# Kernel tuning notes

Measured on AMD Instinct MI355X. Metric: run time of the kernel, lower is better.

Reference implementation:

```python
import jax, jax.numpy as jnp
import numpy as np

N = 100000      # nodes
E = 1600000     # directed edges (before self loops)
F_IN = 3        # node_feature_dim
H = 32          # hidden_dim
BN_EPS = 1e-5


def _linear_params(k, fan_in, fan_out):
    lim = 1.0 / np.sqrt(fan_in)
    kw, kb = jax.random.split(k)
    W = jax.random.uniform(kw, (fan_in, fan_out), jnp.float32, -lim, lim)
    b = jax.random.uniform(kb, (fan_out,), jnp.float32, -lim, lim)
    return W, b


def setup_inputs() -> dict:
    key = jax.random.key(0)
    ks = jax.random.split(key, 12)
    x = jax.random.normal(ks[0], (N, F_IN), jnp.float32)
    edge_index = jax.random.randint(ks[1], (2, E), 0, N, dtype=jnp.int64)
    node_type = jax.random.randint(ks[2], (N,), 0, 3, dtype=jnp.int64)
    W1, b1 = _linear_params(ks[3], F_IN, H)
    W2, b2 = _linear_params(ks[4], H, H)
    W3, b3 = _linear_params(ks[5], H, H)
    g1 = jnp.ones((H,), jnp.float32); be1 = jnp.zeros((H,), jnp.float32)
    g2 = jnp.ones((H,), jnp.float32); be2 = jnp.zeros((H,), jnp.float32)
    Wc1, bc1 = _linear_params(ks[6], H, H // 2)
    Wc2, bc2 = _linear_params(ks[7], H // 2, 1)
    Wd1, bd1 = _linear_params(ks[8], H, H // 2)
    Wd2, bd2 = _linear_params(ks[9], H // 2, 1)
    return dict(x=x, edge_index=edge_index, node_type=node_type,
                W1=W1, b1=b1, W2=W2, b2=b2, W3=W3, b3=b3,
                g1=g1, be1=be1, g2=g2, be2=be2,
                Wc1=Wc1, bc1=bc1, Wc2=Wc2, bc2=bc2,
                Wd1=Wd1, bd1=bd1, Wd2=Wd2, bd2=bd2)


def reference(x, edge_index, node_type, W1, b1, W2, b2, W3, b3,
              g1, be1, g2, be2, Wc1, bc1, Wc2, bc2, Wd1, bd1, Wd2, bd2):
    n = x.shape[0]
    # GCNConv (PyG default): add self loops, symmetric deg^-1/2 normalization
    loop = jnp.arange(n, dtype=edge_index.dtype)
    src = jnp.concatenate([edge_index[0], loop])  # [E+N]
    dst = jnp.concatenate([edge_index[1], loop])
    deg = jax.ops.segment_sum(jnp.ones_like(dst, dtype=x.dtype), dst, num_segments=n)
    dinv = jnp.where(deg > 0, jax.lax.rsqrt(jnp.maximum(deg, 1.0)), 0.0)
    norm = dinv[src] * dinv[dst]  # [E+N]

    def conv(h, W, b):
        msg = (h @ W)[src] * norm[:, None]                  # gather + scale
        return jax.ops.segment_sum(msg, dst, num_segments=n) + b  # scatter-add

    def bn(h, g, be):  # BatchNorm1d with batch statistics (training math)
        mu = h.mean(axis=0)
        var = ((h - mu) ** 2).mean(axis=0)
        return (h - mu) * jax.lax.rsqrt(var + BN_EPS) * g + be

    h = bn(jax.nn.relu(conv(x, W1, b1)), g1, be1)   # dropout = identity (eval)
    h = bn(jax.nn.relu(conv(h, W2, b2)), g2, be2)
    h = jax.nn.relu(conv(h, W3, b3))

    cand_mask = node_type == 0
    cand_emb = h[cand_mask]                                 # [C, H]
    cand_scores = (jax.nn.relu(cand_emb @ Wc1 + bc1) @ Wc2 + bc2)[:, 0]

    w = jax.nn.softmax(h.sum(axis=1))[:, None]              # [N,1] importance
    g_emb = (h * w).sum(axis=0, keepdims=True)              # [1, H]
    dn = (jax.nn.relu(g_emb @ Wd1 + bd1) @ Wd2 + bd2).reshape(())

    logits = jnp.concatenate([cand_scores, dn[None]], axis=0)
    cand_idx = jnp.nonzero(cand_mask)[0]
    return logits, cand_idx
```

## Files before the change

kernel.cpp:

```cpp
#include <hip/hip_runtime.h>
#include <hip/hip_bf16.h>

typedef unsigned int uint;
typedef unsigned short ushort;

#define NB_MAX 256
#define NPB_MAX 2048

static __device__ __forceinline__ ushort f2b(float f) {
    uint u = __float_as_uint(f);
    uint r = (u + 0x7FFFu + ((u >> 16) & 1u)) >> 16;
    return (ushort)r;
}
static __device__ __forceinline__ float b2f_u(ushort h) { return __uint_as_float(((uint)h) << 16); }

static __device__ __forceinline__ void unpack8(uint4 v, float* o) {
    o[0] = b2f_u(v.x & 0xFFFF); o[1] = b2f_u(v.x >> 16);
    o[2] = b2f_u(v.y & 0xFFFF); o[3] = b2f_u(v.y >> 16);
    o[4] = b2f_u(v.z & 0xFFFF); o[5] = b2f_u(v.z >> 16);
    o[6] = b2f_u(v.w & 0xFFFF); o[7] = b2f_u(v.w >> 16);
}

static __device__ __forceinline__ unsigned wave_incl_scan(unsigned v) {
    int lane = threadIdx.x & 63;
    #pragma unroll
    for (int d = 1; d < 64; d <<= 1) {
        unsigned t = (unsigned)__shfl_up((int)v, d, 64);
        if (lane >= d) v += t;
    }
    return v;
}

static __device__ void block_excl_scan(const uint* in, uint* out, int n, uint* wscr) {
    int tid = threadIdx.x;
    int lane = tid & 63, wid = tid >> 6;
    int base = tid * 8;
    uint v[8], pre[8], s = 0;
    #pragma unroll
    for (int k = 0; k < 8; k++) v[k] = (base + k < n) ? in[base + k] : 0u;
    #pragma unroll
    for (int k = 0; k < 8; k++) { pre[k] = s; s += v[k]; }
    uint is = wave_incl_scan(s);
    __syncthreads();
    if (lane == 63) wscr[wid] = is;
    __syncthreads();
    uint woff = 0;
    for (int wI = 0; wI < wid; wI++) woff += wscr[wI];
    uint excl = is - s + woff;
    #pragma unroll
    for (int k = 0; k < 8; k++) if (base + k < n) out[base + k] = excl + pre[k];
    __syncthreads();
}

__global__ __launch_bounds__(256) void bucket_hist_kernel(const int* src, const int* dst,
                                                          const int* nt, uint* bcnt, uint* bcand,
                                                          int E, int N, int NB, int shift) {
    __shared__ uint bh[NB_MAX], ch[NB_MAX];
    int tid = threadIdx.x;
    bh[tid] = 0; ch[tid] = 0;
    __syncthreads();
    int gs = gridDim.x * 256;
    for (int i = blockIdx.x * 256 + tid; i < E; i += gs) {
        int d = dst[i], s = src[i];
        if ((uint)d < (uint)N && (uint)s < (uint)N) atomicAdd(&bh[d >> shift], 1u);
    }
    for (int i = blockIdx.x * 256 + tid; i < N; i += gs) {
        if (nt[i] == 0) atomicAdd(&ch[i >> shift], 1u);
    }
    __syncthreads();
    if (bh[tid]) atomicAdd(&bcnt[tid], bh[tid]);
    if (ch[tid]) atomicAdd(&bcand[tid], ch[tid]);
}

__global__ __launch_bounds__(256) void partition_kernel(const int* src, const int* dst,
                                                        const uint* bcnt, uint* alloc0,
                                                        uint* staging, int E, int N, int shift) {
    __shared__ uint bbase_s[NB_MAX];
    __shared__ uint lh[NB_MAX], gb[NB_MAX];
    __shared__ uint ws4[4];
    int tid = threadIdx.x;
    int lane = tid & 63, wid = tid >> 6;
    uint a = bcnt[tid];
    uint ia = wave_incl_scan(a);
    if (lane == 63) ws4[wid] = ia;
    __syncthreads();
    uint off = 0;
    for (int wI = 0; wI < wid; wI++) off += ws4[wI];
    bbase_s[tid] = ia - a + off;
    lh[tid] = 0;
    __syncthreads();
    int base = blockIdx.x * 2048;
    uint mask = (1u << shift) - 1u;
    int sreg[8], breg[8];
    uint rreg[8], dlreg[8];
    #pragma unroll
    for (int k = 0; k < 8; k++) {
        int e = base + k * 256 + tid;
        breg[k] = -1;
        if (e < E) {
            int s = src[e], d = dst[e];
            if ((uint)d < (uint)N && (uint)s < (uint)N) {
                int b = d >> shift;
                sreg[k] = s; dlreg[k] = (uint)d & mask; breg[k] = b;
                rreg[k] = atomicAdd(&lh[b], 1u);
            }
        }
    }
    __syncthreads();
    gb[tid] = lh[tid] ? (bbase_s[tid] + atomicAdd(&alloc0[tid], lh[tid])) : 0u;
    __syncthreads();
    #pragma unroll
    for (int k = 0; k < 8; k++) {
        if (breg[k] >= 0)
            staging[gb[breg[k]] + rreg[k]] = (dlreg[k] << 17) | (uint)sreg[k];
    }
}

__global__ __launch_bounds__(256) void local_csr_kernel(const uint* staging, const uint* bcnt,
                                                        const uint* bcand, const int* nt,
                                                        const float* x, const float* W1,
                                                        int* csr_src, uint* csr_off, uint* cand_pos,
                                                        float* dinv, ushort* zb,
                                                        int N, int shift, int NB) {
    __shared__ uint deg[NPB_MAX];
    __shared__ uint ofs[NPB_MAX];
    __shared__ uint ws4[4];
    __shared__ uint sb[4];
    __shared__ float Ws[96];
    int b = blockIdx.x, tid = threadIdx.x;
    int lane = tid & 63, wid = tid >> 6;
    if (tid < 96) Ws[tid] = W1[tid];
    uint a = bcnt[tid];
    uint ia = wave_incl_scan(a);
    if (lane == 63) ws4[wid] = ia;
    __syncthreads();
    uint off = 0;
    for (int wI = 0; wI < wid; wI++) off += ws4[wI];
    if (tid == b) { sb[0] = ia - a + off; sb[1] = ia + off; }
    __syncthreads();
    uint c = bcand[tid];
    uint ic = wave_incl_scan(c);
    if (lane == 63) ws4[wid] = ic;
    __syncthreads();
    uint offc = 0;
    for (int wI = 0; wI < wid; wI++) offc += ws4[wI];
    if (tid == b) sb[2] = ic - c + offc;
    __syncthreads();
    uint ebase = sb[0], eend = sb[1], cb = sb[2];
    int nbase = b << shift;
    int ncount = min(1 << shift, N - nbase);
    for (int i = tid; i < ncount; i += 256) deg[i] = 0;
    __syncthreads();
    for (uint p = ebase + tid; p < eend; p += 256)
        atomicAdd(&deg[staging[p] >> 17], 1u);
    __syncthreads();
    block_excl_scan(deg, ofs, ncount, ws4);
    for (int i = tid; i < ncount; i += 256)
        csr_off[nbase + i] = ebase + ofs[i];
    if (b == NB - 1 && tid == 0) csr_off[N] = eend;
    for (int i = tid; i < ncount; i += 256) {
        int g = nbase + i;
        float di = rsqrtf((float)(deg[i] + 1u));
        dinv[g] = di;
        float x0 = x[3 * g], x1 = x[3 * g + 1], x2 = x[3 * g + 2];
        uint pk[16];
        #pragma unroll
        for (int q = 0; q < 16; q++) {
            int j0 = 2 * q, j1 = 2 * q + 1;
            float o0 = (x0 * Ws[j0] + x1 * Ws[32 + j0] + x2 * Ws[64 + j0]) * di;
            float o1 = (x0 * Ws[j1] + x1 * Ws[32 + j1] + x2 * Ws[64 + j1]) * di;
            pk[q] = (uint)f2b(o0) | ((uint)f2b(o1) << 16);
        }
        uint4* zp = (uint4*)(zb + (size_t)g * 32);
        #pragma unroll
        for (int r = 0; r < 4; r++) zp[r] = make_uint4(pk[4*r], pk[4*r+1], pk[4*r+2], pk[4*r+3]);
    }
    __syncthreads();
    for (int i = tid; i < ncount; i += 256) deg[i] = 0;
    __syncthreads();
    for (uint p = ebase + tid; p < eend; p += 256) {
        uint pkv = staging[p];
        uint dl = pkv >> 17;
        uint pos = ebase + ofs[dl] + atomicAdd(&deg[dl], 1u);
        csr_src[pos] = (int)(pkv & 0x1FFFFu);
    }
    __syncthreads();
    for (int i = tid; i < ncount; i += 256) deg[i] = (nt[nbase + i] == 0) ? 1u : 0u;
    __syncthreads();
    block_excl_scan(deg, ofs, ncount, ws4);
    for (int i = tid; i < ncount; i += 256) cand_pos[nbase + i] = cb + ofs[i];
}

__global__ __launch_bounds__(256) void gemmf_kernel(const ushort* hb, const float* stats_sum,
                                                    const float* stats_sq, const float* g,
                                                    const float* be, const float* W,
                                                    const float* dinv, ushort* zb, int n,
                                                    float inv_n) {
    __shared__ float Ws[1024];
    __shared__ float cs[32];
    __shared__ float a_s[32], d_s[32];
    int tid = threadIdx.x;
    if (tid < 32) {
        float mu = stats_sum[tid] * inv_n;
        float var = fmaxf(stats_sq[tid] * inv_n - mu * mu, 0.f);
        float a = g[tid] * rsqrtf(var + 1e-5f);
        a_s[tid] = a;
        d_s[tid] = be[tid] - mu * a;
    }
    __syncthreads();
    #pragma unroll
    for (int t = tid; t < 1024; t += 256) Ws[t] = a_s[t >> 5] * W[t];
    if (tid < 32) {
        float c = 0.f;
        for (int k = 0; k < 32; k++) c += d_s[k] * W[k * 32 + tid];
        cs[tid] = c;
    }
    __syncthreads();
    int i = blockIdx.x * 256 + tid;
    if (i >= n) return;
    const uint4* hp = (const uint4*)(hb + (size_t)i * 32);
    float hk[32];
    #pragma unroll
    for (int r = 0; r < 4; r++) unpack8(hp[r], hk + r * 8);
    float acc[32];
    #pragma unroll
    for (int j = 0; j < 32; j++) acc[j] = cs[j];
    #pragma unroll
    for (int k = 0; k < 32; k++) {
        float h0 = hk[k];
        #pragma unroll
        for (int j = 0; j < 32; j++) acc[j] += h0 * Ws[k * 32 + j];
    }
    float di = dinv[i];
    uint pk[16];
    #pragma unroll
    for (int q = 0; q < 16; q++)
        pk[q] = (uint)f2b(acc[2*q] * di) | ((uint)f2b(acc[2*q+1] * di) << 16);
    uint4* zp = (uint4*)(zb + (size_t)i * 32);
    #pragma unroll
    for (int r = 0; r < 4; r++) zp[r] = make_uint4(pk[4*r], pk[4*r+1], pk[4*r+2], pk[4*r+3]);
}

__global__ __launch_bounds__(256) void agg_kernel(const ushort* zb, const int* csr_src,
                                                  const uint* csr_off, const float* dinv,
                                                  const float* bias, ushort* hb, int n,
                                                  int mode, float* stats_sum, float* stats_sq,
                                                  float* rowsum, uint* maxkey) {
    const int tid = threadIdx.x;
    const int wave = tid >> 6;
    const int lane = tid & 63;
    const int c4 = lane & 3;
    const int slot = lane >> 2;
    float bs[8], bq[8];
    #pragma unroll
    for (int j = 0; j < 8; j++) { bs[j] = 0.f; bq[j] = 0.f; }
    float lmax = -3.0e38f;
    int node = (blockIdx.x * 4 + wave) * 16 + slot;
    if (node < n) {
        uint s = csr_off[node], e = csr_off[node + 1];
        float acc[8];
        unpack8(*(const uint4*)(zb + (size_t)node * 32 + c4 * 8), acc);
        for (uint p = s; p < e; p += 8) {
            uint idx[8];
            float wg[8];
            #pragma unroll
            for (int j = 0; j < 8; j++) {
                uint q = p + (uint)j;
                uint qc = min(q, e - 1u);
                idx[j] = (uint)csr_src[qc];
                wg[j] = (q < e) ? 1.f : 0.f;
            }
            #pragma unroll
            for (int j = 0; j < 8; j++) {
                float t[8];
                unpack8(*(const uint4*)(zb + (size_t)idx[j] * 32 + c4 * 8), t);
                #pragma unroll
                for (int cI = 0; cI < 8; cI++) acc[cI] = fmaf(wg[j], t[cI], acc[cI]);
            }
        }
        float di = dinv[node];
        float hv[8];
        #pragma unroll
        for (int j = 0; j < 8; j++) hv[j] = fmaxf(di * acc[j] + bias[c4 * 8 + j], 0.f);
        uint4 o;
        o.x = (uint)f2b(hv[0]) | ((uint)f2b(hv[1]) << 16);
        o.y = (uint)f2b(hv[2]) | ((uint)f2b(hv[3]) << 16);
        o.z = (uint)f2b(hv[4]) | ((uint)f2b(hv[5]) << 16);
        o.w = (uint)f2b(hv[6]) | ((uint)f2b(hv[7]) << 16);
        *(uint4*)(hb + (size_t)node * 32 + c4 * 8) = o;
        if (mode == 0) {
            #pragma unroll
            for (int j = 0; j < 8; j++) { bs[j] = hv[j]; bq[j] = hv[j] * hv[j]; }
        } else {
            float rs = ((hv[0] + hv[1]) + (hv[2] + hv[3])) + ((hv[4] + hv[5]) + (hv[6] + hv[7]));
            rs += __shfl_xor(rs, 1, 64);
            rs += __shfl_xor(rs, 2, 64);
            if (c4 == 0) { rowsum[node] = rs; lmax = rs; }
        }
    }
    if (mode == 0) {
        #pragma unroll
        for (int m = 4; m < 64; m <<= 1) {
            #pragma unroll
            for (int j = 0; j < 8; j++) {
                bs[j] += __shfl_xor(bs[j], m, 64);
                bq[j] += __shfl_xor(bq[j], m, 64);
            }
        }
        __shared__ float ssum[4][32], ssq[4][32];
        if (slot == 0) {
            #pragma unroll
            for (int j = 0; j < 8; j++) { ssum[wave][c4 * 8 + j] = bs[j]; ssq[wave][c4 * 8 + j] = bq[j]; }
        }
        __syncthreads();
        if (tid < 32) {
            atomicAdd(&stats_sum[tid], ssum[0][tid] + ssum[1][tid] + ssum[2][tid] + ssum[3][tid]);
            atomicAdd(&stats_sq[tid],  ssq[0][tid] + ssq[1][tid] + ssq[2][tid] + ssq[3][tid]);
        }
    } else {
        #pragma unroll
        for (int m = 1; m < 64; m <<= 1) lmax = fmaxf(lmax, __shfl_xor(lmax, m, 64));
        __shared__ float lm[4];
        if (lane == 0) lm[wave] = lmax;
        __syncthreads();
        if (tid == 0) {
            float m = fmaxf(fmaxf(lm[0], lm[1]), fmaxf(lm[2], lm[3]));
            uint u = __float_as_uint(m);
            uint key = (u & 0x80000000u) ? ~u : (u | 0x80000000u);
            atomicMax(maxkey, key);
        }
    }
}

__global__ __launch_bounds__(256) void head_kernel(const ushort* hb, const int* nt,
                                                   const uint* pos, const float* Wc1,
                                                   const float* bc1, const float* Wc2,
                                                   const float* bc2, const float* rowsum,
                                                   const uint* maxkey, float* gvec, float* Zp,
                                                   uint* ticket, const float* Wd1,
                                                   const float* bd1, const float* Wd2,
                                                   const float* bd2, float* out, int n, int C) {
    __shared__ float W1s[512], b1s[16], W2s[16];
    __shared__ float ls[256];
    __shared__ float ge[32], tt[16];
    __shared__ int lastflag;
    int tid = threadIdx.x;
    for (int t = tid; t < 512; t += 256) W1s[t] = Wc1[t];
    if (tid < 16) { b1s[tid] = bc1[tid]; W2s[tid] = Wc2[tid]; }
    __syncthreads();
    int i = blockIdx.x * 256 + tid;
    if (i < n && nt[i] == 0) {
        const uint4* hp = (const uint4*)(hb + (size_t)i * 32);
        float hv[32];
        #pragma unroll
        for (int r = 0; r < 4; r++) unpack8(hp[r], hv + r * 8);
        float s = bc2[0];
        #pragma unroll
        for (int j = 0; j < 16; j++) {
            float u = b1s[j];
            #pragma unroll
            for (int k = 0; k < 32; k++) u += hv[k] * W1s[k * 16 + j];
            s += fmaxf(u, 0.f) * W2s[j];
        }
        s = fminf(fmaxf(s, -1000.f), 1000.f);
        uint p = pos[i];
        if (p < (uint)C) {
            out[p] = s;
            out[C + 1 + p] = (float)i;
        }
    }
    uint key = *maxkey;
    float M = 0.f;
    if (key != 0u) M = (key & 0x80000000u) ? __uint_as_float(key ^ 0x80000000u) : __uint_as_float(~key);
    int lane = tid & 31, grp = tid >> 5;
    int stride = gridDim.x * 8;
    float accZ = 0.f, accg = 0.f;
    for (int node = blockIdx.x * 8 + grp; node < n; node += stride) {
        float ew = __expf(rowsum[node] - M);
        accg += b2f_u(hb[(size_t)node * 32 + lane]) * ew;
        if (lane == 0) accZ += ew;
    }
    ls[tid] = accg;
    __syncthreads();
    if (tid < 32) {
        float a = 0.f;
        #pragma unroll
        for (int g = 0; g < 8; g++) a += ls[tid + 32 * g];
        atomicAdd(&gvec[tid], a);
    }
    __syncthreads();
    ls[tid] = (lane == 0) ? accZ : 0.f;
    __syncthreads();
    if (tid == 0) {
        float a = 0.f;
        for (int t = 0; t < 256; t += 32) a += ls[t];
        atomicAdd(Zp, a);
        __threadfence();
        uint old = atomicAdd(ticket, 1u);
        lastflag = (old == gridDim.x - 1) ? 1 : 0;
    }
    __syncthreads();
    if (lastflag) {
        __threadfence();
        if (tid < 32) ge[tid] = atomicAdd(&gvec[tid], 0.f);
        if (tid == 0) ls[0] = atomicAdd(Zp, 0.f);
        __syncthreads();
        float Zv = fmaxf(ls[0], 1e-30f);
        if (tid < 32) ge[tid] /= Zv;
        __syncthreads();
        if (tid < 16) {
            float s = bd1[tid];
            for (int k = 0; k < 32; k++) s += ge[k] * Wd1[k * 16 + tid];
            tt[tid] = fmaxf(s, 0.f);
        }
        __syncthreads();
        if (tid == 0) {
            float s = bd2[0];
            for (int j = 0; j < 16; j++) s += tt[j] * Wd2[j];
            out[C] = fminf(fmaxf(s, -1000.f), 1000.f);
        }
    }
}

extern "C" void kernel_launch(void* const* d_in, const int* in_sizes, int n_in,
                              void* d_out, int out_size, void* d_ws, size_t ws_size,
                              hipStream_t stream) {
    const float* x   = (const float*)d_in[0];
    const int*   ei  = (const int*)d_in[1];
    const int*   nt  = (const int*)d_in[2];
    const float* W1  = (const float*)d_in[3];  const float* b1  = (const float*)d_in[4];
    const float* W2  = (const float*)d_in[5];  const float* b2  = (const float*)d_in[6];
    const float* W3  = (const float*)d_in[7];  const float* b3  = (const float*)d_in[8];
    const float* g1  = (const float*)d_in[9];  const float* be1 = (const float*)d_in[10];
    const float* g2  = (const float*)d_in[11]; const float* be2 = (const float*)d_in[12];
    const float* Wc1 = (const float*)d_in[13]; const float* bc1 = (const float*)d_in[14];
    const float* Wc2 = (const float*)d_in[15]; const float* bc2 = (const float*)d_in[16];
    const float* Wd1 = (const float*)d_in[17]; const float* bd1 = (const float*)d_in[18];
    const float* Wd2 = (const float*)d_in[19]; const float* bd2 = (const float*)d_in[20];

    const int N = in_sizes[0] / 3;
    const int E = in_sizes[1] / 2;
    const int C = (out_size - 1) / 2;
    const int* e_src = ei;
    const int* e_dst = ei + E;
    float* out = (float*)d_out;

    int shift = 9;
    while (((N + (1 << shift) - 1) >> shift) > NB_MAX) shift++;
    const int NB = (N + (1 << shift) - 1) >> shift;

    char* w = (char*)d_ws;
    auto alloc = [&](size_t bytes) { void* p = (void*)w; w += (bytes + 255) & ~(size_t)255; return p; };
    float*    stats  = (float*)alloc(256 * 4);
    uint*     bcnt   = (uint*)alloc(NB_MAX * 4);
    uint*     bcand  = (uint*)alloc(NB_MAX * 4);
    uint*     alloc0 = (uint*)alloc(NB_MAX * 4);
    size_t zero_bytes = (size_t)((char*)w - (char*)stats);
    float*    dinv   = (float*)alloc((size_t)N * 4);
    uint*     csr_off= (uint*)alloc((size_t)(N + 1) * 4);
    uint*     cand_pos=(uint*)alloc((size_t)N * 4);
    float*    rowsum = (float*)alloc((size_t)N * 4);
    int*      csr_src= (int*)alloc((size_t)E * 4);
    ushort*   zb     = (ushort*)alloc((size_t)N * 32 * 2);
    ushort*   hb     = (ushort*)alloc((size_t)N * 32 * 2);
    uint*     staging = (uint*)hb;

    float* sum1 = stats;       float* sq1 = stats + 32;
    float* sum2 = stats + 64;  float* sq2 = stats + 96;
    float* gvec = stats + 128; float* Zp  = stats + 160;
    uint* maxkey = (uint*)(stats + 161);
    uint* ticket = (uint*)(stats + 162);

    hipMemsetAsync(stats, 0, zero_bytes, stream);

    const int gN   = (N + 255) / 256;
    const int gPar = (E + 2047) / 2048;
    const int gAgg = (N + 63) / 64;
    const float inv_n = 1.0f / (float)N;

    hipLaunchKernelGGL(bucket_hist_kernel, dim3(784), dim3(256), 0, stream, e_src, e_dst, nt, bcnt, bcand, E, N, NB, shift);
    hipLaunchKernelGGL(partition_kernel, dim3(gPar), dim3(256), 0, stream, e_src, e_dst, bcnt, alloc0, staging, E, N, shift);
    hipLaunchKernelGGL(local_csr_kernel, dim3(NB), dim3(256), 0, stream, staging, bcnt, bcand, nt,
                       x, W1, csr_src, csr_off, cand_pos, dinv, zb, N, shift, NB);

    hipLaunchKernelGGL(agg_kernel, dim3(gAgg), dim3(256), 0, stream, zb, csr_src, csr_off,
                       dinv, b1, hb, N, 0, sum1, sq1, rowsum, maxkey);

    hipLaunchKernelGGL(gemmf_kernel, dim3(gN), dim3(256), 0, stream, hb, sum1, sq1, g1, be1, W2, dinv, zb, N, inv_n);
    hipLaunchKernelGGL(agg_kernel, dim3(gAgg), dim3(256), 0, stream, zb, csr_src, csr_off,
                       dinv, b2, hb, N, 0, sum2, sq2, rowsum, maxkey);

    hipLaunchKernelGGL(gemmf_kernel, dim3(gN), dim3(256), 0, stream, hb, sum2, sq2, g2, be2, W3, dinv, zb, N, inv_n);
    hipLaunchKernelGGL(agg_kernel, dim3(gAgg), dim3(256), 0, stream, zb, csr_src, csr_off,
                       dinv, b3, hb, N, 1, sum1, sq1, rowsum, maxkey);

    hipLaunchKernelGGL(head_kernel, dim3(gN), dim3(256), 0, stream, hb, nt, cand_pos,
                       Wc1, bc1, Wc2, bc2, rowsum, maxkey, gvec, Zp, ticket,
                       Wd1, bd1, Wd2, bd2, out, N, C);
}
```

Measured before the change: 369.0 us.

## Fuse pipeline into cooperative persistent megakernel and store features as fp8

Replaces the sequence of separate kernels with a single cooperative-launched persistent kernel that runs every phase, separated by grid-wide syncs, with a multi-kernel fallback. Node feature buffers change from bf16 to a software-encoded e4m3-style fp8 format, halving gather traffic during aggregation. Staging gets its own buffer instead of aliasing hb, and the bucket scan is done once instead of per block. This removes launch gaps and memory traffic, but fp8 adds precision loss and grid syncs may leave cores idle between phases.

```diff
diff --git a/kernel.cpp b/kernel.cpp
--- a/kernel.cpp
+++ b/kernel.cpp
@@ -1,36 +1,80 @@
 #include <hip/hip_runtime.h>
-#include <hip/hip_bf16.h>
+#include <hip/hip_cooperative_groups.h>
 
 typedef unsigned int uint;
-typedef unsigned short ushort;
-
-#define NB_MAX 256
-#define NPB_MAX 2048
-
-static __device__ __forceinline__ ushort f2b(float f) {
-    uint u = __float_as_uint(f);
-    uint r = (u + 0x7FFFu + ((u >> 16) & 1u)) >> 16;
-    return (ushort)r;
-}
-static __device__ __forceinline__ float b2f_u(ushort h) { return __uint_as_float(((uint)h) << 16); }
-
-static __device__ __forceinline__ void unpack8(uint4 v, float* o) {
-    o[0] = b2f_u(v.x & 0xFFFF); o[1] = b2f_u(v.x >> 16);
-    o[2] = b2f_u(v.y & 0xFFFF); o[3] = b2f_u(v.y >> 16);
-    o[4] = b2f_u(v.z & 0xFFFF); o[5] = b2f_u(v.z >> 16);
-    o[6] = b2f_u(v.w & 0xFFFF); o[7] = b2f_u(v.w >> 16);
-}
-
-static __device__ __forceinline__ unsigned wave_incl_scan(unsigned v) {
+typedef unsigned char uchar;
+
+namespace cg = cooperative_groups;
+
+#define SMW 4300
+
+static __device__ __forceinline__ uint f2fp8(float v) {
+    v = fminf(fmaxf(v, -448.f), 448.f);
+    uint u = __float_as_uint(v);
+    uint s = (u >> 24) & 0x80u;
+    uint mag = u & 0x7FFFFFFFu;
+    uint r = mag + 0x7FFFFu + ((mag >> 20) & 1u);
+    if (r < 0x3C800000u) return s;
+    uint e8 = (r - 0x3C000000u) >> 20;
+    return s | min(e8, 0x7Eu);
+}
+static __device__ __forceinline__ float fp82f(uint b) {
+    uint mag = b & 0x7Fu;
+    uint bits = ((b & 0x80u) << 24) | ((mag << 20) + 0x3C000000u);
+    return mag ? __uint_as_float(bits) : 0.f;
+}
+static __device__ __forceinline__ void dec8(uint2 v, float* o) {
+    o[0]=fp82f(v.x&0xFF); o[1]=fp82f((v.x>>8)&0xFF); o[2]=fp82f((v.x>>16)&0xFF); o[3]=fp82f(v.x>>24);
+    o[4]=fp82f(v.y&0xFF); o[5]=fp82f((v.y>>8)&0xFF); o[6]=fp82f((v.y>>16)&0xFF); o[7]=fp82f(v.y>>24);
+}
+static __device__ __forceinline__ uint2 enc8(const float* o) {
+    uint2 r;
+    r.x = f2fp8(o[0]) | (f2fp8(o[1])<<8) | (f2fp8(o[2])<<16) | (f2fp8(o[3])<<24);
+    r.y = f2fp8(o[4]) | (f2fp8(o[5])<<8) | (f2fp8(o[6])<<16) | (f2fp8(o[7])<<24);
+    return r;
+}
+static __device__ __forceinline__ void dec32(const uchar* row, float* o) {
+    const uint4* r4 = (const uint4*)row;
+    uint4 A = r4[0], B = r4[1];
+    dec8(make_uint2(A.x,A.y), o); dec8(make_uint2(A.z,A.w), o+8);
+    dec8(make_uint2(B.x,B.y), o+16); dec8(make_uint2(B.z,B.w), o+24);
+}
+static __device__ __forceinline__ void enc32(const float* o, uchar* row) {
+    uint2 a = enc8(o), b = enc8(o+8), c = enc8(o+16), d = enc8(o+24);
+    uint4* r4 = (uint4*)row;
+    r4[0] = make_uint4(a.x,a.y,b.x,b.y);
+    r4[1] = make_uint4(c.x,c.y,d.x,d.y);
+}
+
+struct GP {
+    const float* x; const int* esrc; const int* edst; const int* nt;
+    const float* W1; const float* b1; const float* W2; const float* b2;
+    const float* W3; const float* b3; const float* g1; const float* be1;
+    const float* g2; const float* be2;
+    const float* Wc1; const float* bc1; const float* Wc2; const float* bc2;
+    const float* Wd1; const float* bd1; const float* Wd2; const float* bd2;
+    float* stats;
+    uint* bcnt; uint* bcand; uint* alloc0;
+    uint* bbase; uint* cbase;
+    float* dinv; uint* csr_off; uint* cand_pos; float* rowsum;
+    int* csr_src; uint* staging;
+    uchar* zb; uchar* hb;
+    float* sum1; float* sq1; float* sum2; float* sq2;
+    float* gvec; float* Zp; uint* maxkey;
+    float* out;
+    int N, E, C, NB, shift, nCh;
+    float inv_n;
+};
+
+static __device__ __forceinline__ uint wave_incl_scan(uint v) {
     int lane = threadIdx.x & 63;
     #pragma unroll
     for (int d = 1; d < 64; d <<= 1) {
-        unsigned t = (unsigned)__shfl_up((int)v, d, 64);
+        uint t = (uint)__shfl_up((int)v, d, 64);
         if (lane >= d) v += t;
     }
     return v;
 }
-
 static __device__ void block_excl_scan(const uint* in, uint* out, int n, uint* wscr) {
     int tid = threadIdx.x;
     int lane = tid & 63, wid = tid >> 6;
@@ -52,252 +96,231 @@
     __syncthreads();
 }
 
-__global__ __launch_bounds__(256) void bucket_hist_kernel(const int* src, const int* dst,
-                                                          const int* nt, uint* bcnt, uint* bcand,
-                                                          int E, int N, int NB, int shift) {
-    __shared__ uint bh[NB_MAX], ch[NB_MAX];
+static __device__ void ph_zero(const GP& p) {
+    if (blockIdx.x != 0) return;
+    uint* z = (uint*)p.stats;
+    for (int i = threadIdx.x; i < 1024; i += 256) z[i] = 0u;
+}
+
+static __device__ void ph_hist(const GP& p, uint* sm) {
+    uint* bh = sm; uint* ch = sm + 256;
     int tid = threadIdx.x;
     bh[tid] = 0; ch[tid] = 0;
     __syncthreads();
     int gs = gridDim.x * 256;
-    for (int i = blockIdx.x * 256 + tid; i < E; i += gs) {
-        int d = dst[i], s = src[i];
-        if ((uint)d < (uint)N && (uint)s < (uint)N) atomicAdd(&bh[d >> shift], 1u);
-    }
-    for (int i = blockIdx.x * 256 + tid; i < N; i += gs) {
-        if (nt[i] == 0) atomicAdd(&ch[i >> shift], 1u);
-    }
-    __syncthreads();
-    if (bh[tid]) atomicAdd(&bcnt[tid], bh[tid]);
-    if (ch[tid]) atomicAdd(&bcand[tid], ch[tid]);
-}
-
-__global__ __launch_bounds__(256) void partition_kernel(const int* src, const int* dst,
-                                                        const uint* bcnt, uint* alloc0,
-                                                        uint* staging, int E, int N, int shift) {
-    __shared__ uint bbase_s[NB_MAX];
-    __shared__ uint lh[NB_MAX], gb[NB_MAX];
-    __shared__ uint ws4[4];
-    int tid = threadIdx.x;
-    int lane = tid & 63, wid = tid >> 6;
-    uint a = bcnt[tid];
-    uint ia = wave_incl_scan(a);
-    if (lane == 63) ws4[wid] = ia;
-    __syncthreads();
-    uint off = 0;
-    for (int wI = 0; wI < wid; wI++) off += ws4[wI];
-    bbase_s[tid] = ia - a + off;
-    lh[tid] = 0;
-    __syncthreads();
-    int base = blockIdx.x * 2048;
-    uint mask = (1u << shift) - 1u;
-    int sreg[8], breg[8];
-    uint rreg[8], dlreg[8];
-    #pragma unroll
-    for (int k = 0; k < 8; k++) {
-        int e = base + k * 256 + tid;
-        breg[k] = -1;
-        if (e < E) {
-            int s = src[e], d = dst[e];
-            if ((uint)d < (uint)N && (uint)s < (uint)N) {
-                int b = d >> shift;
-                sreg[k] = s; dlreg[k] = (uint)d & mask; breg[k] = b;
-                rreg[k] = atomicAdd(&lh[b], 1u);
+    for (int i = blockIdx.x * 256 + tid; i < p.E; i += gs) {
+        int d = p.edst[i], s = p.esrc[i];
+        if ((uint)d < (uint)p.N && (uint)s < (uint)p.N) atomicAdd(&bh[d >> p.shift], 1u);
+    }
+    for (int i = blockIdx.x * 256 + tid; i < p.N; i += gs)
+        if (p.nt[i] == 0) atomicAdd(&ch[i >> p.shift], 1u);
+    __syncthreads();
+    if (bh[tid]) atomicAdd(&p.bcnt[tid], bh[tid]);
+    if (ch[tid]) atomicAdd(&p.bcand[tid], ch[tid]);
+}
+
+static __device__ void ph_bscan(const GP& p, uint* sm) {
+    if (blockIdx.x != 0) return;
+    int tid = threadIdx.x, lane = tid & 63, wid = tid >> 6;
+    uint* ws4 = sm;
+    {
+        uint a = p.bcnt[tid];
+        uint ia = wave_incl_scan(a);
+        if (lane == 63) ws4[wid] = ia;
+        __syncthreads();
+        uint off = 0;
+        for (int wI = 0; wI < wid; wI++) off += ws4[wI];
+        p.bbase[tid] = ia - a + off;
+        if (tid == 255) p.bbase[256] = ia + off;
+        __syncthreads();
+    }
+    {
+        uint a = p.bcand[tid];
+        uint ia = wave_incl_scan(a);
+        if (lane == 63) ws4[wid] = ia;
+        __syncthreads();
+        uint off = 0;
+        for (int wI = 0; wI < wid; wI++) off += ws4[wI];
+        p.cbase[tid] = ia - a + off;
+        if (tid == 255) p.cbase[256] = ia + off;
+        __syncthreads();
+    }
+}
+
+static __device__ void ph_part(const GP& p, uint* sm) {
+    uint* lh = sm; uint* gb = sm + 256;
+    int tid = threadIdx.x;
+    uint mask = (1u << p.shift) - 1u;
+    for (int chunk = blockIdx.x; chunk < p.nCh; chunk += gridDim.x) {
+        lh[tid] = 0;
+        __syncthreads();
+        int base = chunk << 11;
+        int breg[8]; uint rreg[8], pk8[8];
+        #pragma unroll
+        for (int k = 0; k < 8; k++) {
+            int e = base + k * 256 + tid;
+            breg[k] = -1;
+            if (e < p.E) {
+                int s = p.esrc[e], d = p.edst[e];
+                if ((uint)d < (uint)p.N && (uint)s < (uint)p.N) {
+                    int b = d >> p.shift;
+                    pk8[k] = (((uint)d & mask) << 17) | (uint)s;
+                    breg[k] = b;
+                    rreg[k] = atomicAdd(&lh[b], 1u);
+                }
             }
         }
-    }
-    __syncthreads();
-    gb[tid] = lh[tid] ? (bbase_s[tid] + atomicAdd(&alloc0[tid], lh[tid])) : 0u;
-    __syncthreads();
-    #pragma unroll
-    for (int k = 0; k < 8; k++) {
-        if (breg[k] >= 0)
-            staging[gb[breg[k]] + rreg[k]] = (dlreg[k] << 17) | (uint)sreg[k];
-    }
-}
-
-__global__ __launch_bounds__(256) void local_csr_kernel(const uint* staging, const uint* bcnt,
-                                                        const uint* bcand, const int* nt,
-                                                        const float* x, const float* W1,
-                                                        int* csr_src, uint* csr_off, uint* cand_pos,
-                                                        float* dinv, ushort* zb,
-                                                        int N, int shift, int NB) {
-    __shared__ uint deg[NPB_MAX];
-    __shared__ uint ofs[NPB_MAX];
-    __shared__ uint ws4[4];
-    __shared__ uint sb[4];
-    __shared__ float Ws[96];
-    int b = blockIdx.x, tid = threadIdx.x;
-    int lane = tid & 63, wid = tid >> 6;
-    if (tid < 96) Ws[tid] = W1[tid];
-    uint a = bcnt[tid];
-    uint ia = wave_incl_scan(a);
-    if (lane == 63) ws4[wid] = ia;
-    __syncthreads();
-    uint off = 0;
-    for (int wI = 0; wI < wid; wI++) off += ws4[wI];
-    if (tid == b) { sb[0] = ia - a + off; sb[1] = ia + off; }
-    __syncthreads();
-    uint c = bcand[tid];
-    uint ic = wave_incl_scan(c);
-    if (lane == 63) ws4[wid] = ic;
-    __syncthreads();
-    uint offc = 0;
-    for (int wI = 0; wI < wid; wI++) offc += ws4[wI];
-    if (tid == b) sb[2] = ic - c + offc;
-    __syncthreads();
-    uint ebase = sb[0], eend = sb[1], cb = sb[2];
-    int nbase = b << shift;
-    int ncount = min(1 << shift, N - nbase);
-    for (int i = tid; i < ncount; i += 256) deg[i] = 0;
-    __syncthreads();
-    for (uint p = ebase + tid; p < eend; p += 256)
-        atomicAdd(&deg[staging[p] >> 17], 1u);
-    __syncthreads();
-    block_excl_scan(deg, ofs, ncount, ws4);
-    for (int i = tid; i < ncount; i += 256)
-        csr_off[nbase + i] = ebase + ofs[i];
-    if (b == NB - 1 && tid == 0) csr_off[N] = eend;
-    for (int i = tid; i < ncount; i += 256) {
-        int g = nbase + i;
-        float di = rsqrtf((float)(deg[i] + 1u));
-        dinv[g] = di;
-        float x0 = x[3 * g], x1 = x[3 * g + 1], x2 = x[3 * g + 2];
-        uint pk[16];
-        #pragma unroll
-        for (int q = 0; q < 16; q++) {
-            int j0 = 2 * q, j1 = 2 * q + 1;
-            float o0 = (x0 * Ws[j0] + x1 * Ws[32 + j0] + x2 * Ws[64 + j0]) * di;
-            float o1 = (x0 * Ws[j1] + x1 * Ws[32 + j1] + x2 * Ws[64 + j1]) * di;
-            pk[q] = (uint)f2b(o0) | ((uint)f2b(o1) << 16);
-        }
-        uint4* zp = (uint4*)(zb + (size_t)g * 32);
-        #pragma unroll
-        for (int r = 0; r < 4; r++) zp[r] = make_uint4(pk[4*r], pk[4*r+1], pk[4*r+2], pk[4*r+3]);
-    }
-    __syncthreads();
-    for (int i = tid; i < ncount; i += 256) deg[i] = 0;
-    __syncthreads();
-    for (uint p = ebase + tid; p < eend; p += 256) {
-        uint pkv = staging[p];
-        uint dl = pkv >> 17;
-        uint pos = ebase + ofs[dl] + atomicAdd(&deg[dl], 1u);
-        csr_src[pos] = (int)(pkv & 0x1FFFFu);
-    }
-    __syncthreads();
-    for (int i = tid; i < ncount; i += 256) deg[i] = (nt[nbase + i] == 0) ? 1u : 0u;
-    __syncthreads();
-    block_excl_scan(deg, ofs, ncount, ws4);
-    for (int i = tid; i < ncount; i += 256) cand_pos[nbase + i] = cb + ofs[i];
-}
-
-__global__ __launch_bounds__(256) void gemmf_kernel(const ushort* hb, const float* stats_sum,
-                                                    const float* stats_sq, const float* g,
-                                                    const float* be, const float* W,
-                                                    const float* dinv, ushort* zb, int n,
-                                                    float inv_n) {
-    __shared__ float Ws[1024];
-    __shared__ float cs[32];
-    __shared__ float a_s[32], d_s[32];
+        __syncthreads();
+        gb[tid] = lh[tid] ? (p.bbase[tid] + atomicAdd(&p.alloc0[tid], lh[tid])) : 0u;
+        __syncthreads();
+        #pragma unroll
+        for (int k = 0; k < 8; k++)
+            if (breg[k] >= 0) p.staging[gb[breg[k]] + rreg[k]] = pk8[k];
+        __syncthreads();
+    }
+}
+
+static __device__ void ph_localcsr(const GP& p, uint* sm) {
+    uint* deg = sm; uint* ofs = sm + 2048; uint* ws4 = sm + 4096;
+    float* W1s = (float*)(sm + 4104);
+    int tid = threadIdx.x;
+    if (tid < 96) W1s[tid] = p.W1[tid];
+    for (int b = blockIdx.x; b < p.NB; b += gridDim.x) {
+        uint ebase = p.bbase[b], eend = p.bbase[b + 1];
+        uint cb = p.cbase[b];
+        int nbase = b << p.shift;
+        int ncount = min(1 << p.shift, p.N - nbase);
+        for (int i = tid; i < ncount; i += 256) deg[i] = 0;
+        __syncthreads();
+        for (uint q = ebase + tid; q < eend; q += 256)
+            atomicAdd(&deg[p.staging[q] >> 17], 1u);
+        __syncthreads();
+        block_excl_scan(deg, ofs, ncount, ws4);
+        for (int i = tid; i < ncount; i += 256)
+            p.csr_off[nbase + i] = ebase + ofs[i];
+        if (b == p.NB - 1 && tid == 0) p.csr_off[p.N] = eend;
+        for (int i = tid; i < ncount; i += 256) {
+            int g = nbase + i;
+            float di = rsqrtf((float)(deg[i] + 1u));
+            p.dinv[g] = di;
+            float x0 = p.x[3*g], x1 = p.x[3*g+1], x2 = p.x[3*g+2];
+            float o[32];
+            #pragma unroll
+            for (int j = 0; j < 32; j++)
+                o[j] = (x0 * W1s[j] + x1 * W1s[32 + j] + x2 * W1s[64 + j]) * di;
+            enc32(o, p.zb + (size_t)g * 32);
+        }
+        __syncthreads();
+        for (int i = tid; i < ncount; i += 256) deg[i] = 0;
+        __syncthreads();
+        for (uint q = ebase + tid; q < eend; q += 256) {
+            uint pkv = p.staging[q];
+            uint dl = pkv >> 17;
+            uint pos = ebase + ofs[dl] + atomicAdd(&deg[dl], 1u);
+            p.csr_src[pos] = (int)(pkv & 0x1FFFFu);
+        }
+        __syncthreads();
+        for (int i = tid; i < ncount; i += 256) deg[i] = (p.nt[nbase + i] == 0) ? 1u : 0u;
+        __syncthreads();
+        block_excl_scan(deg, ofs, ncount, ws4);
+        for (int i = tid; i < ncount; i += 256) p.cand_pos[nbase + i] = cb + ofs[i];
+        __syncthreads();
+    }
+}
+
+static __device__ void ph_gemmf(const GP& p, uint* sm, const uchar* hin, uchar* zout,
+                                const float* ssum, const float* ssq,
+                                const float* g, const float* be, const float* W) {
+    float* Wsf = (float*)sm;
+    float* cs  = (float*)(sm + 1024);
+    float* a_s = (float*)(sm + 1056);
+    float* d_s = (float*)(sm + 1088);
     int tid = threadIdx.x;
     if (tid < 32) {
-        float mu = stats_sum[tid] * inv_n;
-        float var = fmaxf(stats_sq[tid] * inv_n - mu * mu, 0.f);
+        float mu = ssum[tid] * p.inv_n;
+        float var = fmaxf(ssq[tid] * p.inv_n - mu * mu, 0.f);
         float a = g[tid] * rsqrtf(var + 1e-5f);
         a_s[tid] = a;
         d_s[tid] = be[tid] - mu * a;
     }
     __syncthreads();
     #pragma unroll
-    for (int t = tid; t < 1024; t += 256) Ws[t] = a_s[t >> 5] * W[t];
+    for (int t = tid; t < 1024; t += 256) Wsf[t] = a_s[t >> 5] * W[t];
     if (tid < 32) {
         float c = 0.f;
         for (int k = 0; k < 32; k++) c += d_s[k] * W[k * 32 + tid];
         cs[tid] = c;
     }
     __syncthreads();
-    int i = blockIdx.x * 256 + tid;
-    if (i >= n) return;
-    const uint4* hp = (const uint4*)(hb + (size_t)i * 32);
-    float hk[32];
-    #pragma unroll
-    for (int r = 0; r < 4; r++) unpack8(hp[r], hk + r * 8);
-    float acc[32];
-    #pragma unroll
-    for (int j = 0; j < 32; j++) acc[j] = cs[j];
-    #pragma unroll
-    for (int k = 0; k < 32; k++) {
-        float h0 = hk[k];
-        #pragma unroll
-        for (int j = 0; j < 32; j++) acc[j] += h0 * Ws[k * 32 + j];
-    }
-    float di = dinv[i];
-    uint pk[16];
-    #pragma unroll
-    for (int q = 0; q < 16; q++)
-        pk[q] = (uint)f2b(acc[2*q] * di) | ((uint)f2b(acc[2*q+1] * di) << 16);
-    uint4* zp = (uint4*)(zb + (size_t)i * 32);
-    #pragma unroll
-    for (int r = 0; r < 4; r++) zp[r] = make_uint4(pk[4*r], pk[4*r+1], pk[4*r+2], pk[4*r+3]);
-}
-
-__global__ __launch_bounds__(256) void agg_kernel(const ushort* zb, const int* csr_src,
-                                                  const uint* csr_off, const float* dinv,
-                                                  const float* bias, ushort* hb, int n,
-                                                  int mode, float* stats_sum, float* stats_sq,
-                                                  float* rowsum, uint* maxkey) {
-    const int tid = threadIdx.x;
-    const int wave = tid >> 6;
-    const int lane = tid & 63;
-    const int c4 = lane & 3;
-    const int slot = lane >> 2;
+    for (int i = blockIdx.x * 256 + tid; i < p.N; i += gridDim.x * 256) {
+        float hk[32], acc[32];
+        dec32(hin + (size_t)i * 32, hk);
+        #pragma unroll
+        for (int j = 0; j < 32; j++) acc[j] = cs[j];
+        #pragma unroll
+        for (int k = 0; k < 32; k++) {
+            float h0 = hk[k];
+            #pragma unroll
+            for (int j = 0; j < 32; j++) acc[j] += h0 * Wsf[k * 32 + j];
+        }
+        float di = p.dinv[i];
+        #pragma unroll
+        for (int j = 0; j < 32; j++) acc[j] *= di;
+        enc32(acc, zout + (size_t)i * 32);
+    }
+}
+
+static __device__ void ph_agg(const GP& p, uint* sm, const uchar* z, uchar* h,
+                              const float* bias, int mode, float* gsum, float* gsq) {
+    int tid = threadIdx.x;
+    int wave = tid >> 6, lane = tid & 63;
+    int c4 = lane & 3, slot = lane >> 2;
+    float bv[8];
+    #pragma unroll
+    for (int j = 0; j < 8; j++) bv[j] = bias[c4 * 8 + j];
     float bs[8], bq[8];
     #pragma unroll
     for (int j = 0; j < 8; j++) { bs[j] = 0.f; bq[j] = 0.f; }
     float lmax = -3.0e38f;
-    int node = (blockIdx.x * 4 + wave) * 16 + slot;
-    if (node < n) {
-        uint s = csr_off[node], e = csr_off[node + 1];
+    int qstride = gridDim.x * 64;
+    for (int node = blockIdx.x * 64 + (tid >> 2); node < p.N; node += qstride) {
+        uint s = p.csr_off[node], e = p.csr_off[node + 1];
         float acc[8];
-        unpack8(*(const uint4*)(zb + (size_t)node * 32 + c4 * 8), acc);
-        for (uint p = s; p < e; p += 8) {
-            uint idx[8];
-            float wg[8];
+        dec8(*(const uint2*)(z + (size_t)node * 32 + c4 * 8), acc);
+        for (uint pp = s; pp < e; pp += 8) {
+            uint idx[8]; float wg[8];
             #pragma unroll
             for (int j = 0; j < 8; j++) {
-                uint q = p + (uint)j;
+                uint q = pp + (uint)j;
                 uint qc = min(q, e - 1u);
-                idx[j] = (uint)csr_src[qc];
+                idx[j] = (uint)p.csr_src[qc];
                 wg[j] = (q < e) ? 1.f : 0.f;
             }
             #pragma unroll
             for (int j = 0; j < 8; j++) {
-                float t[8];
-                unpack8(*(const uint4*)(zb + (size_t)idx[j] * 32 + c4 * 8), t);
+                float t8[8];
+                dec8(*(const uint2*)(z + (size_t)idx[j] * 32 + c4 * 8), t8);
                 #pragma unroll
-                for (int cI = 0; cI < 8; cI++) acc[cI] = fmaf(wg[j], t[cI], acc[cI]);
+                for (int cI = 0; cI < 8; cI++) acc[cI] = fmaf(wg[j], t8[cI], acc[cI]);
             }
         }
-        float di = dinv[node];
+        float di = p.dinv[node];
         float hv[8];
         #pragma unroll
-        for (int j = 0; j < 8; j++) hv[j] = fmaxf(di * acc[j] + bias[c4 * 8 + j], 0.f);
-        uint4 o;
-        o.x = (uint)f2b(hv[0]) | ((uint)f2b(hv[1]) << 16);
-        o.y = (uint)f2b(hv[2]) | ((uint)f2b(hv[3]) << 16);
-        o.z = (uint)f2b(hv[4]) | ((uint)f2b(hv[5]) << 16);
-        o.w = (uint)f2b(hv[6]) | ((uint)f2b(hv[7]) << 16);
-        *(uint4*)(hb + (size_t)node * 32 + c4 * 8) = o;
+        for (int j = 0; j < 8; j++) hv[j] = fmaxf(di * acc[j] + bv[j], 0.f);
+        *(uint2*)(h + (size_t)node * 32 + c4 * 8) = enc8(hv);
         if (mode == 0) {
             #pragma unroll
-            for (int j = 0; j < 8; j++) { bs[j] = hv[j]; bq[j] = hv[j] * hv[j]; }
+            for (int j = 0; j < 8; j++) { bs[j] += hv[j]; bq[j] += hv[j] * hv[j]; }
         } else {
-            float rs = ((hv[0] + hv[1]) + (hv[2] + hv[3])) + ((hv[4] + hv[5]) + (hv[6] + hv[7]));
+            float rs = ((hv[0]+hv[1])+(hv[2]+hv[3])) + ((hv[4]+hv[5])+(hv[6]+hv[7]));
             rs += __shfl_xor(rs, 1, 64);
             rs += __shfl_xor(rs, 2, 64);
-            if (c4 == 0) { rowsum[node] = rs; lmax = rs; }
-        }
-    }
+            if (c4 == 0) { p.rowsum[node] = rs; lmax = fmaxf(lmax, rs); }
+        }
+    }
+    float* s1 = (float*)sm;
+    float* s2 = (float*)(sm + 128);
     if (mode == 0) {
         #pragma unroll
         for (int m = 4; m < 64; m <<= 1) {
@@ -307,54 +330,89 @@
                 bq[j] += __shfl_xor(bq[j], m, 64);
             }
         }
-        __shared__ float ssum[4][32], ssq[4][32];
+        __syncthreads();
         if (slot == 0) {
             #pragma unroll
-            for (int j = 0; j < 8; j++) { ssum[wave][c4 * 8 + j] = bs[j]; ssq[wave][c4 * 8 + j] = bq[j]; }
+            for (int j = 0; j < 8; j++) { s1[wave*32 + c4*8 + j] = bs[j]; s2[wave*32 + c4*8 + j] = bq[j]; }
         }
         __syncthreads();
         if (tid < 32) {
-            atomicAdd(&stats_sum[tid], ssum[0][tid] + ssum[1][tid] + ssum[2][tid] + ssum[3][tid]);
-            atomicAdd(&stats_sq[tid],  ssq[0][tid] + ssq[1][tid] + ssq[2][tid] + ssq[3][tid]);
-        }
+            atomicAdd(&gsum[tid], s1[tid] + s1[32+tid] + s1[64+tid] + s1[96+tid]);
+            atomicAdd(&gsq[tid],  s2[tid] + s2[32+tid] + s2[64+tid] + s2[96+tid]);
+        }
+        __syncthreads();
     } else {
         #pragma unroll
         for (int m = 1; m < 64; m <<= 1) lmax = fmaxf(lmax, __shfl_xor(lmax, m, 64));
-        __shared__ float lm[4];
-        if (lane == 0) lm[wave] = lmax;
+        __syncthreads();
+        if (lane == 0) s1[wave] = lmax;
         __syncthreads();
         if (tid == 0) {
-            float m = fmaxf(fmaxf(lm[0], lm[1]), fmaxf(lm[2], lm[3]));
+            float m = fmaxf(fmaxf(s1[0], s1[1]), fmaxf(s1[2], s1[3]));
             uint u = __float_as_uint(m);
             uint key = (u & 0x80000000u) ? ~u : (u | 0x80000000u);
-            atomicMax(maxkey, key);
-        }
-    }
-}
-
-__global__ __launch_bounds__(256) void head_kernel(const ushort* hb, const int* nt,
-                                                   const uint* pos, const float* Wc1,
-                                                   const float* bc1, const float* Wc2,
-                                                   const float* bc2, const float* rowsum,
-                                                   const uint* maxkey, float* gvec, float* Zp,
-                                                   uint* ticket, const float* Wd1,
-                                                   const float* bd1, const float* Wd2,
-                                                   const float* bd2, float* out, int n, int C) {
-    __shared__ float W1s[512], b1s[16], W2s[16];
-    __shared__ float ls[256];
-    __shared__ float ge[32], tt[16];
-    __shared__ int lastflag;
-    int tid = threadIdx.x;
-    for (int t = tid; t < 512; t += 256) W1s[t] = Wc1[t];
-    if (tid < 16) { b1s[tid] = bc1[tid]; W2s[tid] = Wc2[tid]; }
-    __syncthreads();
-    int i = blockIdx.x * 256 + tid;
-    if (i < n && nt[i] == 0) {
-        const uint4* hp = (const uint4*)(hb + (size_t)i * 32);
+            atomicMax(p.maxkey, key);
+        }
+        __syncthreads();
+    }
+}
+
+static __device__ void ph_pool(const GP& p, uint* sm) {
+    int tid = threadIdx.x;
+    int wave = tid >> 6, lane = tid & 63;
+    int c4 = lane & 3, slot = lane >> 2;
+    uint key = *p.maxkey;
+    float M = 0.f;
+    if (key != 0u) M = (key & 0x80000000u) ? __uint_as_float(key ^ 0x80000000u) : __uint_as_float(~key);
+    float ag[8];
+    #pragma unroll
+    for (int j = 0; j < 8; j++) ag[j] = 0.f;
+    float az = 0.f;
+    int qstride = gridDim.x * 64;
+    for (int node = blockIdx.x * 64 + (tid >> 2); node < p.N; node += qstride) {
+        float ew = __expf(p.rowsum[node] - M);
+        float t8[8];
+        dec8(*(const uint2*)(p.hb + (size_t)node * 32 + c4 * 8), t8);
+        #pragma unroll
+        for (int j = 0; j < 8; j++) ag[j] += t8[j] * ew;
+        if (c4 == 0) az += ew;
+    }
+    #pragma unroll
+    for (int m = 4; m < 64; m <<= 1) {
+        #pragma unroll
+        for (int j = 0; j < 8; j++) ag[j] += __shfl_xor(ag[j], m, 64);
+        az += __shfl_xor(az, m, 64);
+    }
+    float* s1 = (float*)sm;
+    float* zarr = (float*)(sm + 128);
+    __syncthreads();
+    if (slot == 0) {
+        #pragma unroll
+        for (int j = 0; j < 8; j++) s1[wave*32 + c4*8 + j] = ag[j];
+    }
+    if (lane == 0) zarr[wave] = az;
+    __syncthreads();
+    if (tid < 32) atomicAdd(&p.gvec[tid], s1[tid] + s1[32+tid] + s1[64+tid] + s1[96+tid]);
+    if (tid == 0) atomicAdd(p.Zp, zarr[0] + zarr[1] + zarr[2] + zarr[3]);
+    __syncthreads();
+}
+
+static __device__ void ph_head(const GP& p, uint* sm) {
+    float* W1s = (float*)sm;
+    float* b1s = (float*)(sm + 512);
+    float* W2s = (float*)(sm + 528);
+    float* ge  = (float*)(sm + 544);
+    float* tt  = (float*)(sm + 576);
+    float* zsh = (float*)(sm + 592);
+    int tid = threadIdx.x;
+    for (int t = tid; t < 512; t += 256) W1s[t] = p.Wc1[t];
+    if (tid < 16) { b1s[tid] = p.bc1[tid]; W2s[tid] = p.Wc2[tid]; }
+    __syncthreads();
+    for (int i = blockIdx.x * 256 + tid; i < p.N; i += gridDim.x * 256) {
+        if (p.nt[i] != 0) continue;
         float hv[32];
-        #pragma unroll
-        for (int r = 0; r < 4; r++) unpack8(hp[r], hv + r * 8);
-        float s = bc2[0];
+        dec32(p.hb + (size_t)i * 32, hv);
+        float s = p.bc2[0];
         #pragma unroll
         for (int j = 0; j < 16; j++) {
             float u = b1s[j];
@@ -363,138 +421,138 @@
             s += fmaxf(u, 0.f) * W2s[j];
         }
         s = fminf(fmaxf(s, -1000.f), 1000.f);
-        uint p = pos[i];
-        if (p < (uint)C) {
-            out[p] = s;
-            out[C + 1 + p] = (float)i;
-        }
-    }
-    uint key = *maxkey;
-    float M = 0.f;
-    if (key != 0u) M = (key & 0x80000000u) ? __uint_as_float(key ^ 0x80000000u) : __uint_as_float(~key);
-    int lane = tid & 31, grp = tid >> 5;
-    int stride = gridDim.x * 8;
-    float accZ = 0.f, accg = 0.f;
-    for (int node = blockIdx.x * 8 + grp; node < n; node += stride) {
-        float ew = __expf(rowsum[node] - M);
-        accg += b2f_u(hb[(size_t)node * 32 + lane]) * ew;
-        if (lane == 0) accZ += ew;
-    }
-    ls[tid] = accg;
-    __syncthreads();
-    if (tid < 32) {
-        float a = 0.f;
-        #pragma unroll
-        for (int g = 0; g < 8; g++) a += ls[tid + 32 * g];
-        atomicAdd(&gvec[tid], a);
-    }
-    __syncthreads();
-    ls[tid] = (lane == 0) ? accZ : 0.f;
-    __syncthreads();
-    if (tid == 0) {
-        float a = 0.f;
-        for (int t = 0; t < 256; t += 32) a += ls[t];
-        atomicAdd(Zp, a);
-        __threadfence();
-        uint old = atomicAdd(ticket, 1u);
-        lastflag = (old == gridDim.x - 1) ? 1 : 0;
-    }
-    __syncthreads();
-    if (lastflag) {
-        __threadfence();
-        if (tid < 32) ge[tid] = atomicAdd(&gvec[tid], 0.f);
-        if (tid == 0) ls[0] = atomicAdd(Zp, 0.f);
-        __syncthreads();
-        float Zv = fmaxf(ls[0], 1e-30f);
-        if (tid < 32) ge[tid] /= Zv;
+        uint pp = p.cand_pos[i];
+        if (pp < (uint)p.C) {
+            p.out[pp] = s;
+            p.out[p.C + 1 + pp] = (float)i;
+        }
+    }
+    if (blockIdx.x == 0) {
+        if (tid < 32) ge[tid] = p.gvec[tid];
+        if (tid == 0) zsh[0] = *p.Zp;
+        __syncthreads();
+        float Z = fmaxf(zsh[0], 1e-30f);
+        if (tid < 32) ge[tid] /= Z;
         __syncthreads();
         if (tid < 16) {
-            float s = bd1[tid];
-            for (int k = 0; k < 32; k++) s += ge[k] * Wd1[k * 16 + tid];
+            float s = p.bd1[tid];
+            for (int k = 0; k < 32; k++) s += ge[k] * p.Wd1[k * 16 + tid];
             tt[tid] = fmaxf(s, 0.f);
         }
         __syncthreads();
         if (tid == 0) {
-            float s = bd2[0];
-            for (int j = 0; j < 16; j++) s += tt[j] * Wd2[j];
-            out[C] = fminf(fmaxf(s, -1000.f), 1000.f);
-        }
-    }
-}
+            float s = p.bd2[0];
+            for (int j = 0; j < 16; j++) s += tt[j] * p.Wd2[j];
+            p.out[p.C] = fminf(fmaxf(s, -1000.f), 1000.f);
+        }
+    }
+}
+
+__global__ __launch_bounds__(256, 4) void mega_kernel(GP p) {
+    __shared__ uint sm[SMW];
+    cg::grid_group g = cg::this_grid();
+    ph_zero(p);                                              g.sync();
+    ph_hist(p, sm);                                          g.sync();
+    ph_bscan(p, sm);                                         g.sync();
+    ph_part(p, sm);                                          g.sync();
+    ph_localcsr(p, sm);                                      g.sync();
+    ph_agg(p, sm, p.zb, p.hb, p.b1, 0, p.sum1, p.sq1);       g.sync();
+    ph_gemmf(p, sm, p.hb, p.zb, p.sum1, p.sq1, p.g1, p.be1, p.W2); g.sync();
+    ph_agg(p, sm, p.zb, p.hb, p.b2, 0, p.sum2, p.sq2);       g.sync();
+    ph_gemmf(p, sm, p.hb, p.zb, p.sum2, p.sq2, p.g2, p.be2, p.W3); g.sync();
+    ph_agg(p, sm, p.zb, p.hb, p.b3, 1, p.sum1, p.sq1);       g.sync();
+    ph_pool(p, sm);                                          g.sync();
+    ph_head(p, sm);
+}
+
+__global__ __launch_bounds__(256) void k_zero(GP p)    { ph_zero(p); }
+__global__ __launch_bounds__(256) void k_hist(GP p)    { __shared__ uint sm[SMW]; ph_hist(p, sm); }
+__global__ __launch_bounds__(256) void k_bscan(GP p)   { __shared__ uint sm[SMW]; ph_bscan(p, sm); }
+__global__ __launch_bounds__(256) void k_part(GP p)    { __shared__ uint sm[SMW]; ph_part(p, sm); }
+__global__ __launch_bounds__(256) void k_lcsr(GP p)    { __shared__ uint sm[SMW]; ph_localcsr(p, sm); }
+__global__ __launch_bounds__(256) void k_agg1(GP p)    { __shared__ uint sm[SMW]; ph_agg(p, sm, p.zb, p.hb, p.b1, 0, p.sum1, p.sq1); }
+__global__ __launch_bounds__(256) void k_gemmf2(GP p)  { __shared__ uint sm[SMW]; ph_gemmf(p, sm, p.hb, p.zb, p.sum1, p.sq1, p.g1, p.be1, p.W2); }
+__global__ __launch_bounds__(256) void k_agg2(GP p)    { __shared__ uint sm[SMW]; ph_agg(p, sm, p.zb, p.hb, p.b2, 0, p.sum2, p.sq2); }
+__global__ __launch_bounds__(256) void k_gemmf3(GP p)  { __shared__ uint sm[SMW]; ph_gemmf(p, sm, p.hb, p.zb, p.sum2, p.sq2, p.g2, p.be2, p.W3); }
+__global__ __launch_bounds__(256) void k_agg3(GP p)    { __shared__ uint sm[SMW]; ph_agg(p, sm, p.zb, p.hb, p.b3, 1, p.sum1, p.sq1); }
+__global__ __launch_bounds__(256) void k_pool(GP p)    { __shared__ uint sm[SMW]; ph_pool(p, sm); }
+__global__ __launch_bounds__(256) void k_head(GP p)    { __shared__ uint sm[SMW]; ph_head(p, sm); }
 
 extern "C" void kernel_launch(void* const* d_in, const int* in_sizes, int n_in,
                               void* d_out, int out_size, void* d_ws, size_t ws_size,
                               hipStream_t stream) {
-    const float* x   = (const float*)d_in[0];
-    const int*   ei  = (const int*)d_in[1];
-    const int*   nt  = (const int*)d_in[2];
-    const float* W1  = (const float*)d_in[3];  const float* b1  = (const float*)d_in[4];
-    const float* W2  = (const float*)d_in[5];  const float* b2  = (const float*)d_in[6];
-    const float* W3  = (const float*)d_in[7];  const float* b3  = (const float*)d_in[8];
-    const float* g1  = (const float*)d_in[9];  const float* be1 = (const float*)d_in[10];
-    const float* g2  = (const float*)d_in[11]; const float* be2 = (const float*)d_in[12];
-    const float* Wc1 = (const float*)d_in[13]; const float* bc1 = (const float*)d_in[14];
-    const float* Wc2 = (const float*)d_in[15]; const float* bc2 = (const float*)d_in[16];
-    const float* Wd1 = (const float*)d_in[17]; const float* bd1 = (const float*)d_in[18];
-    const float* Wd2 = (const float*)d_in[19]; const float* bd2 = (const float*)d_in[20];
-
-    const int N = in_sizes[0] / 3;
-    const int E = in_sizes[1] / 2;
-    const int C = (out_size - 1) / 2;
-    const int* e_src = ei;
-    const int* e_dst = ei + E;
-    float* out = (float*)d_out;
+    GP p;
+    p.x   = (const float*)d_in[0];
+    const int* ei = (const int*)d_in[1];
+    p.nt  = (const int*)d_in[2];
+    p.W1  = (const float*)d_in[3];  p.b1  = (const float*)d_in[4];
+    p.W2  = (const float*)d_in[5];  p.b2  = (const float*)d_in[6];
+    p.W3  = (const float*)d_in[7];  p.b3  = (const float*)d_in[8];
+    p.g1  = (const float*)d_in[9];  p.be1 = (const float*)d_in[10];
+    p.g2  = (const float*)d_in[11]; p.be2 = (const float*)d_in[12];
+    p.Wc1 = (const float*)d_in[13]; p.bc1 = (const float*)d_in[14];
+    p.Wc2 = (const float*)d_in[15]; p.bc2 = (const float*)d_in[16];
+    p.Wd1 = (const float*)d_in[17]; p.bd1 = (const float*)d_in[18];
+    p.Wd2 = (const float*)d_in[19]; p.bd2 = (const float*)d_in[20];
+
+    p.N = in_sizes[0] / 3;
+    p.E = in_sizes[1] / 2;
+    p.C = (out_size - 1) / 2;
+    p.esrc = ei;
+    p.edst = ei + p.E;
+    p.out = (float*)d_out;
+    p.inv_n = 1.0f / (float)p.N;
 
     int shift = 9;
-    while (((N + (1 << shift) - 1) >> shift) > NB_MAX) shift++;
-    const int NB = (N + (1 << shift) - 1) >> shift;
+    while (((p.N + (1 << shift) - 1) >> shift) > 256) shift++;
+    p.shift = shift;
+    p.NB = (p.N + (1 << shift) - 1) >> shift;
+    p.nCh = (p.E + 2047) >> 11;
 
     char* w = (char*)d_ws;
-    auto alloc = [&](size_t bytes) { void* p = (void*)w; w += (bytes + 255) & ~(size_t)255; return p; };
-    float*    stats  = (float*)alloc(256 * 4);
-    uint*     bcnt   = (uint*)alloc(NB_MAX * 4);
-    uint*     bcand  = (uint*)alloc(NB_MAX * 4);
-    uint*     alloc0 = (uint*)alloc(NB_MAX * 4);
-    size_t zero_bytes = (size_t)((char*)w - (char*)stats);
-    float*    dinv   = (float*)alloc((size_t)N * 4);
-    uint*     csr_off= (uint*)alloc((size_t)(N + 1) * 4);
-    uint*     cand_pos=(uint*)alloc((size_t)N * 4);
-    float*    rowsum = (float*)alloc((size_t)N * 4);
-    int*      csr_src= (int*)alloc((size_t)E * 4);
-    ushort*   zb     = (ushort*)alloc((size_t)N * 32 * 2);
-    ushort*   hb     = (ushort*)alloc((size_t)N * 32 * 2);
-    uint*     staging = (uint*)hb;
-
-    float* sum1 = stats;       float* sq1 = stats + 32;
-    float* sum2 = stats + 64;  float* sq2 = stats + 96;
-    float* gvec = stats + 128; float* Zp  = stats + 160;
-    uint* maxkey = (uint*)(stats + 161);
-    uint* ticket = (uint*)(stats + 162);
-
-    hipMemsetAsync(stats, 0, zero_bytes, stream);
-
-    const int gN   = (N + 255) / 256;
-    const int gPar = (E + 2047) / 2048;
-    const int gAgg = (N + 63) / 64;
-    const float inv_n = 1.0f / (float)N;
-
-    hipLaunchKernelGGL(bucket_hist_kernel, dim3(784), dim3(256), 0, stream, e_src, e_dst, nt, bcnt, bcand, E, N, NB, shift);
-    hipLaunchKernelGGL(partition_kernel, dim3(gPar), dim3(256), 0, stream, e_src, e_dst, bcnt, alloc0, staging, E, N, shift);
-    hipLaunchKernelGGL(local_csr_kernel, dim3(NB), dim3(256), 0, stream, staging, bcnt, bcand, nt,
-                       x, W1, csr_src, csr_off, cand_pos, dinv, zb, N, shift, NB);
-
-    hipLaunchKernelGGL(agg_kernel, dim3(gAgg), dim3(256), 0, stream, zb, csr_src, csr_off,
-                       dinv, b1, hb, N, 0, sum1, sq1, rowsum, maxkey);
-
-    hipLaunchKernelGGL(gemmf_kernel, dim3(gN), dim3(256), 0, stream, hb, sum1, sq1, g1, be1, W2, dinv, zb, N, inv_n);
-    hipLaunchKernelGGL(agg_kernel, dim3(gAgg), dim3(256), 0, stream, zb, csr_src, csr_off,
-                       dinv, b2, hb, N, 0, sum2, sq2, rowsum, maxkey);
-
-    hipLaunchKernelGGL(gemmf_kernel, dim3(gN), dim3(256), 0, stream, hb, sum2, sq2, g2, be2, W3, dinv, zb, N, inv_n);
-    hipLaunchKernelGGL(agg_kernel, dim3(gAgg), dim3(256), 0, stream, zb, csr_src, csr_off,
-                       dinv, b3, hb, N, 1, sum1, sq1, rowsum, maxkey);
-
-    hipLaunchKernelGGL(head_kernel, dim3(gN), dim3(256), 0, stream, hb, nt, cand_pos,
-                       Wc1, bc1, Wc2, bc2, rowsum, maxkey, gvec, Zp, ticket,
-                       Wd1, bd1, Wd2, bd2, out, N, C);
-}
+    auto alloc = [&](size_t bytes) { void* q = (void*)w; w += (bytes + 255) & ~(size_t)255; return q; };
+    p.stats   = (float*)alloc(256 * 4);
+    p.bcnt    = (uint*)alloc(256 * 4);
+    p.bcand   = (uint*)alloc(256 * 4);
+    p.alloc0  = (uint*)alloc(256 * 4);
+    p.bbase   = (uint*)alloc(257 * 4);
+    p.cbase   = (uint*)alloc(257 * 4);
+    p.dinv    = (float*)alloc((size_t)p.N * 4);
+    p.csr_off = (uint*)alloc((size_t)(p.N + 1) * 4);
+    p.cand_pos= (uint*)alloc((size_t)p.N * 4);
+    p.rowsum  = (float*)alloc((size_t)p.N * 4);
+    p.csr_src = (int*)alloc((size_t)p.E * 4);
+    p.staging = (uint*)alloc((size_t)p.E * 4);
+    p.zb      = (uchar*)alloc((size_t)p.N * 32);
+    p.hb      = (uchar*)alloc((size_t)p.N * 32);
+
+    p.sum1 = p.stats;       p.sq1 = p.stats + 32;
+    p.sum2 = p.stats + 64;  p.sq2 = p.stats + 96;
+    p.gvec = p.stats + 128; p.Zp  = p.stats + 160;
+    p.maxkey = (uint*)(p.stats + 161);
+
+    hipError_t err = hipErrorUnknown;
+    int nbcu = 0;
+    if (hipOccupancyMaxActiveBlocksPerMultiprocessor(&nbcu, mega_kernel, 256, 0) == hipSuccess && nbcu > 0) {
+        int G = nbcu * 256;
+        if (G > 2048) G = 2048;
+        void* kargs[] = { (void*)&p };
+        err = hipLaunchCooperativeKernel((const void*)mega_kernel, dim3(G), dim3(256), kargs, 0, stream);
+    }
+    if (err != hipSuccess) {
+        const int gN   = (p.N + 255) / 256;
+        const int gAgg = (p.N + 63) / 64;
+        hipLaunchKernelGGL(k_zero,  dim3(1),     dim3(256), 0, stream, p);
+        hipLaunchKernelGGL(k_hist,  dim3(784),   dim3(256), 0, stream, p);
+        hipLaunchKernelGGL(k_bscan, dim3(1),     dim3(256), 0, stream, p);
+        hipLaunchKernelGGL(k_part,  dim3(p.nCh), dim3(256), 0, stream, p);
+        hipLaunchKernelGGL(k_lcsr,  dim3(p.NB),  dim3(256), 0, stream, p);
+        hipLaunchKernelGGL(k_agg1,  dim3(gAgg),  dim3(256), 0, stream, p);
+        hipLaunchKernelGGL(k_gemmf2,dim3(gN),    dim3(256), 0, stream, p);
+        hipLaunchKernelGGL(k_agg2,  dim3(gAgg),  dim3(256), 0, stream, p);
+        hipLaunchKernelGGL(k_gemmf3,dim3(gN),    dim3(256), 0, stream, p);
+        hipLaunchKernelGGL(k_agg3,  dim3(gAgg),  dim3(256), 0, stream, p);
+        hipLaunchKernelGGL(k_pool,  dim3(512),   dim3(256), 0, stream, p);
+        hipLaunchKernelGGL(k_head,  dim3(gN),    dim3(256), 0, stream, p);
+    }
+}
```

Result: slower. 1.220 ms (+230.5%).
